# Kernel tuning notes

Hardware: AMD Instinct MI355X
Metric: run time of the kernel (lower is better)

The kernel has to match this reference:

```python
import jax, jax.numpy as jnp
import numpy as np

STRIDE = 1
PADDING = 1

def setup_inputs() -> dict:
    key = jax.random.key(0)
    k1, k2, k3 = jax.random.split(key, 3)
    x = jax.random.normal(k1, (32, 64, 112, 112), dtype=jnp.float32)
    weight = jax.random.normal(k2, (128, 64, 3, 3), dtype=jnp.float32)
    bias = jax.random.normal(k3, (128,), dtype=jnp.float32)
    return {"x": x, "weight": weight, "bias": bias}

def reference(x, weight, bias):
    # Equivalent of the explicit-loop conv: standard cross-correlation conv2d
    # x: [N, C, H, W], weight: [O, C, KH, KW] -> out: [N, O, OH, OW]
    out = jax.lax.conv_general_dilated(
        x, weight,
        window_strides=(STRIDE, STRIDE),
        padding=[(PADDING, PADDING), (PADDING, PADDING)],
        dimension_numbers=("NCHW", "OIHW", "NCHW"),
    )
    return out + bias[None, :, None, None]
```

## Files before the change

kernel.cpp:

```cpp
#include <hip/hip_runtime.h>

#define CIN 64
#define OC 128
#define HW 112
#define HWHW (HW*HW)
#define NIMG 32

#define XN_ELEMS (NIMG*HWHW*CIN)
#define WT_OFF_EL (XN_ELEMS + 128)

#define ROWE (114*64)

typedef __attribute__((ext_vector_type(8))) short short8;
typedef __attribute__((ext_vector_type(4))) float floatx4;

__device__ inline unsigned short f2bf(float f) {
    unsigned u = __float_as_uint(f);
    u += 0x7fffu + ((u >> 16) & 1u);
    return (unsigned short)(u >> 16);
}

__device__ inline void async16(const unsigned short* g, unsigned short* l) {
    __builtin_amdgcn_global_load_lds(
        (const __attribute__((address_space(1))) void*)g,
        (__attribute__((address_space(3))) void*)l, 16, 0, 0);
}

__global__ __launch_bounds__(256) void xform_x(const float* __restrict__ x,
                                               unsigned short* __restrict__ xws)
{
    __shared__ float s[HW * (CIN + 1)];
    const int tid = threadIdx.x;
    const int n = blockIdx.x / HW;
    const int h = blockIdx.x % HW;

    const float* xp = x + (size_t)n * CIN * HWHW + h * HW;
    for (int idx = tid; idx < CIN * HW; idx += 256) {
        int c = idx / HW;
        int w = idx - c * HW;
        s[w * (CIN + 1) + c] = xp[c * HWHW + w];
    }
    __syncthreads();

    unsigned short* op = xws + ((size_t)(n * HW + h)) * HW * CIN;
    for (int idx = tid; idx < (CIN * HW) / 8; idx += 256) {
        int w  = idx >> 3;
        int c0 = (idx & 7) * 8;
        union { unsigned short us[8]; uint4 v; } u;
        #pragma unroll
        for (int j = 0; j < 8; ++j)
            u.us[j] = f2bf(s[w * (CIN + 1) + c0 + j]);
        *(uint4*)(op + w * CIN + c0) = u.v;
    }
}

__global__ __launch_bounds__(256) void xform_w(const float* __restrict__ wgt,
                                               unsigned short* __restrict__ ws16)
{
    const int idx = blockIdx.x * 256 + threadIdx.x;
    const int c = idx & 63;
    const int o = (idx >> 6) & 127;
    const int t = idx >> 13;
    const float v = wgt[(o * CIN + c) * 9 + t];
    ws16[WT_OFF_EL + ((size_t)(t * 2 + (c >> 5)) * 128 + o) * 32 + (c & 31)] = f2bf(v);
}

__global__ __launch_bounds__(256, 2) void conv_mfma(
    const unsigned short* __restrict__ ws16,
    const float* __restrict__ bias,
    float* __restrict__ out)
{
    __shared__ unsigned short sx[4 * ROWE];

    const int tid  = threadIdx.x;
    const int wave = tid >> 6;
    const int lane = tid & 63;
    const int lane_lo = lane & 15;
    const int lane_hi = lane >> 4;

    const int bid = blockIdx.x;
    const int n   = bid / 56;
    const int rp  = bid % 56;
    const int h0  = rp * 2;

    {
        const int slot = wave;
        const int hr = h0 + slot - 1;
        unsigned short* rowb = sx + slot * ROWE;
        if ((unsigned)hr < (unsigned)HW) {
            if (lane < 8)        *(uint4*)(rowb + lane * 8) = (uint4){0,0,0,0};
            else if (lane < 16)  *(uint4*)(rowb + 113*64 + (lane - 8) * 8) = (uint4){0,0,0,0};
            const unsigned short* gr = ws16 + ((size_t)(n * HW + hr)) * HW * CIN;
            const int grp = lane >> 3;
            const int sub = lane & 7;
            const int swz = sub ^ ((1 + grp) & 7);
            const unsigned short* gl = gr + grp * 64 + swz * 8;
            #pragma unroll
            for (int j = 0; j < 14; ++j)
                async16(gl + j * 512, rowb + (1 + j * 8) * 64);
        } else {
            #pragma unroll
            for (int t = 0; t < 14; ++t)
                *(uint4*)(rowb + t * 512 + lane * 8) = (uint4){0,0,0,0};
            if (lane < 16) *(uint4*)(rowb + 7168 + lane * 8) = (uint4){0,0,0,0};
        }
    }
    __syncthreads();

    floatx4 acc[7][4];
    #pragma unroll
    for (int mt = 0; mt < 7; ++mt)
        #pragma unroll
        for (int ot = 0; ot < 4; ++ot)
            acc[mt][ot] = (floatx4){0.f, 0.f, 0.f, 0.f};

    const unsigned short* wA = ws16 + WT_OFF_EL;
    const int row_idx = wave >> 1;
    const int o0 = (wave & 1) * 64;
    const int aL = (o0 + lane_lo) * 32 + lane_hi * 8;

    short8 a[2][2][4];
    #pragma unroll
    for (int k01 = 0; k01 < 2; ++k01)
        #pragma unroll
        for (int ot = 0; ot < 4; ++ot)
            a[0][k01][ot] = *(const short8*)(wA + k01 * 4096 + ot * 512 + aL);

    #pragma unroll
    for (int tap = 0; tap < 9; ++tap) {
        const int dh = tap / 3 - 1;
        const int dw = tap % 3 - 1;
        const int cur = tap & 1, nxt = cur ^ 1;
        if (tap < 8) {
            #pragma unroll
            for (int k01 = 0; k01 < 2; ++k01)
                #pragma unroll
                for (int ot = 0; ot < 4; ++ot)
                    a[nxt][k01][ot] = *(const short8*)(
                        wA + ((tap + 1) * 2 + k01) * 4096 + ot * 512 + aL);
        }
        const int colL = lane_lo + dw + 1;
        const unsigned short* sb = sx + (row_idx + 1 + dh) * ROWE + colL * 64;
        const int sw0 = (lane_hi ^ (colL & 7)) * 8;
        const int sw1 = ((lane_hi + 4) ^ (colL & 7)) * 8;

        #pragma unroll
        for (int mt = 0; mt < 7; ++mt) {
            const short8 b0 = *(const short8*)(sb + mt * 1024 + sw0);
            const short8 b1 = *(const short8*)(sb + mt * 1024 + sw1);
            #pragma unroll
            for (int ot = 0; ot < 4; ++ot)
                acc[mt][ot] = __builtin_amdgcn_mfma_f32_16x16x32_bf16(
                    a[cur][0][ot], b0, acc[mt][ot], 0, 0, 0);
            #pragma unroll
            for (int ot = 0; ot < 4; ++ot)
                acc[mt][ot] = __builtin_amdgcn_mfma_f32_16x16x32_bf16(
                    a[cur][1][ot], b1, acc[mt][ot], 0, 0, 0);
        }
    }

    const int h = h0 + row_idx;
    #pragma unroll
    for (int ot = 0; ot < 4; ++ot) {
        const int ob = o0 + ot * 16 + lane_hi * 4;
        const float4 bv = *(const float4*)(bias + ob);
        #pragma unroll
        for (int mt = 0; mt < 7; ++mt) {
            const int w = mt * 16 + lane_lo;
            float* op = out + ((size_t)(n * OC + ob) * HW + h) * HW + w;
            op[0]        = acc[mt][ot].x + bv.x;
            op[HWHW]     = acc[mt][ot].y + bv.y;
            op[2 * HWHW] = acc[mt][ot].z + bv.z;
            op[3 * HWHW] = acc[mt][ot].w + bv.w;
        }
    }
}

extern "C" void kernel_launch(void* const* d_in, const int* in_sizes, int n_in,
                              void* d_out, int out_size, void* d_ws, size_t ws_size,
                              hipStream_t stream) {
    const float* x    = (const float*)d_in[0];
    const float* wgt  = (const float*)d_in[1];
    const float* bias = (const float*)d_in[2];
    float* out = (float*)d_out;
    unsigned short* ws16 = (unsigned short*)d_ws;

    hipLaunchKernelGGL(xform_x, dim3(NIMG * HW), dim3(256), 0, stream, x, ws16);
    hipLaunchKernelGGL(xform_w, dim3(288), dim3(256), 0, stream, wgt, ws16);
    hipLaunchKernelGGL(conv_mfma, dim3(NIMG * 56), dim3(256), 0, stream,
                       ws16, bias, out);
}
```

Baseline: 332.2 us.

## Process four rows per block with a ring buffer and overlap staging with compute

Each conv block now computes four output rows in two passes over a five-slot LDS ring, so the six input rows it needs are staged once instead of the eight staged by two two-row blocks. The next row's async load and the stores of the first pass run alongside the second pass. Other changes: the x and weight transforms merge into one launch, x reads use float2, block IDs are remapped, and output writes use nontemporal stores. The larger LDS footprint may reduce occupancy, and the extra barriers add synchronisation cost.

```diff
diff --git a/kernel.cpp b/kernel.cpp
--- a/kernel.cpp
+++ b/kernel.cpp
@@ -10,6 +10,7 @@
 #define WT_OFF_EL (XN_ELEMS + 128)
 
 #define ROWE (114*64)
+#define NSLOT 5
 
 typedef __attribute__((ext_vector_type(8))) short short8;
 typedef __attribute__((ext_vector_type(4))) float floatx4;
@@ -26,43 +27,142 @@
         (__attribute__((address_space(3))) void*)l, 16, 0, 0);
 }
 
-__global__ __launch_bounds__(256) void xform_x(const float* __restrict__ x,
-                                               unsigned short* __restrict__ xws)
-{
-    __shared__ float s[HW * (CIN + 1)];
+__global__ __launch_bounds__(256) void xform(const float* __restrict__ x,
+                                             const float* __restrict__ wgt,
+                                             unsigned short* __restrict__ ws16)
+{
     const int tid = threadIdx.x;
-    const int n = blockIdx.x / HW;
-    const int h = blockIdx.x % HW;
-
-    const float* xp = x + (size_t)n * CIN * HWHW + h * HW;
-    for (int idx = tid; idx < CIN * HW; idx += 256) {
-        int c = idx / HW;
-        int w = idx - c * HW;
-        s[w * (CIN + 1) + c] = xp[c * HWHW + w];
-    }
-    __syncthreads();
-
-    unsigned short* op = xws + ((size_t)(n * HW + h)) * HW * CIN;
-    for (int idx = tid; idx < (CIN * HW) / 8; idx += 256) {
-        int w  = idx >> 3;
-        int c0 = (idx & 7) * 8;
-        union { unsigned short us[8]; uint4 v; } u;
-        #pragma unroll
-        for (int j = 0; j < 8; ++j)
-            u.us[j] = f2bf(s[w * (CIN + 1) + c0 + j]);
-        *(uint4*)(op + w * CIN + c0) = u.v;
-    }
-}
-
-__global__ __launch_bounds__(256) void xform_w(const float* __restrict__ wgt,
-                                               unsigned short* __restrict__ ws16)
-{
-    const int idx = blockIdx.x * 256 + threadIdx.x;
-    const int c = idx & 63;
-    const int o = (idx >> 6) & 127;
-    const int t = idx >> 13;
-    const float v = wgt[(o * CIN + c) * 9 + t];
-    ws16[WT_OFF_EL + ((size_t)(t * 2 + (c >> 5)) * 128 + o) * 32 + (c & 31)] = f2bf(v);
+    if (blockIdx.x < NIMG * HW) {
+        __shared__ float s[HW * (CIN + 1)];
+        const int n = blockIdx.x / HW;
+        const int h = blockIdx.x % HW;
+        const float* xp = x + (size_t)n * CIN * HWHW + h * HW;
+        for (int idx = tid; idx < CIN * 56; idx += 256) {
+            const int c  = idx / 56;
+            const int w2 = idx - c * 56;
+            const float2 v = *(const float2*)(xp + c * HWHW + w2 * 2);
+            s[(w2 * 2 + 0) * (CIN + 1) + c] = v.x;
+            s[(w2 * 2 + 1) * (CIN + 1) + c] = v.y;
+        }
+        __syncthreads();
+        unsigned short* op = ws16 + (size_t)(n * HW + h) * HW * CIN;
+        for (int idx = tid; idx < (CIN * HW) / 8; idx += 256) {
+            const int w  = idx >> 3;
+            const int c0 = (idx & 7) * 8;
+            union { unsigned short us[8]; uint4 v; } u;
+            #pragma unroll
+            for (int j = 0; j < 8; ++j)
+                u.us[j] = f2bf(s[w * (CIN + 1) + c0 + j]);
+            *(uint4*)(op + w * CIN + c0) = u.v;
+        }
+    } else {
+        const int idx = (blockIdx.x - NIMG * HW) * 256 + tid;
+        const int c = idx & 63;
+        const int o = (idx >> 6) & 127;
+        const int t = idx >> 13;
+        const float v = wgt[(o * CIN + c) * 9 + t];
+        ws16[WT_OFF_EL + ((size_t)(t * 2 + (c >> 5)) * 128 + o) * 32 + (c & 31)] = f2bf(v);
+    }
+}
+
+__device__ __forceinline__ void stage_row_all(unsigned short* rowb,
+                                              const unsigned short* gr,
+                                              int wave, int lane)
+{
+    if (gr) {
+        const int grp = lane >> 3;
+        const int sub = lane & 7;
+        const int swz = sub ^ ((1 + grp) & 7);
+        const unsigned short* gl = gr + grp * 64 + swz * 8;
+        #pragma unroll
+        for (int k = 0; k < 4; ++k) {
+            const int j = wave + 4 * k;
+            if (j < 14) async16(gl + j * 512, rowb + (1 + j * 8) * 64);
+        }
+        if (wave == 2 && lane < 8) *(uint4*)(rowb + lane * 8) = (uint4){0,0,0,0};
+        if (wave == 3 && lane < 8) *(uint4*)(rowb + 113 * 64 + lane * 8) = (uint4){0,0,0,0};
+    } else {
+        const int t = wave * 64 + lane;
+        #pragma unroll
+        for (int k = 0; k < 4; ++k) {
+            const int e = t + k * 256;
+            if (e < ROWE / 8) *(uint4*)(rowb + e * 8) = (uint4){0,0,0,0};
+        }
+    }
+}
+
+template<int T>
+__device__ __forceinline__ void tile_compute(floatx4 acc[7][4],
+    const unsigned short* __restrict__ wA, const unsigned short* sx,
+    int row_idx, int lane_lo, int lane_hi, int aL)
+{
+    #pragma unroll
+    for (int mt = 0; mt < 7; ++mt)
+        #pragma unroll
+        for (int ot = 0; ot < 4; ++ot)
+            acc[mt][ot] = (floatx4){0.f, 0.f, 0.f, 0.f};
+
+    short8 a[2][2][4];
+    #pragma unroll
+    for (int k01 = 0; k01 < 2; ++k01)
+        #pragma unroll
+        for (int ot = 0; ot < 4; ++ot)
+            a[0][k01][ot] = *(const short8*)(wA + k01 * 4096 + ot * 512 + aL);
+
+    #pragma unroll
+    for (int tap = 0; tap < 9; ++tap) {
+        const int dh = tap / 3 - 1;
+        const int dw = tap % 3 - 1;
+        const int cur = tap & 1, nxt = cur ^ 1;
+        if (tap < 8) {
+            #pragma unroll
+            for (int k01 = 0; k01 < 2; ++k01)
+                #pragma unroll
+                for (int ot = 0; ot < 4; ++ot)
+                    a[nxt][k01][ot] = *(const short8*)(
+                        wA + ((tap + 1) * 2 + k01) * 4096 + ot * 512 + aL);
+        }
+        int slot = row_idx + (1 + dh + 2 * T);
+        if (slot >= NSLOT) slot -= NSLOT;
+        const int colL = lane_lo + dw + 1;
+        const unsigned short* sb = sx + slot * ROWE + colL * 64;
+        const int sw0 = (lane_hi ^ (colL & 7)) * 8;
+        const int sw1 = ((lane_hi + 4) ^ (colL & 7)) * 8;
+
+        #pragma unroll
+        for (int mt = 0; mt < 7; ++mt) {
+            const short8 b0 = *(const short8*)(sb + mt * 1024 + sw0);
+            const short8 b1 = *(const short8*)(sb + mt * 1024 + sw1);
+            #pragma unroll
+            for (int ot = 0; ot < 4; ++ot)
+                acc[mt][ot] = __builtin_amdgcn_mfma_f32_16x16x32_bf16(
+                    a[cur][0][ot], b0, acc[mt][ot], 0, 0, 0);
+            #pragma unroll
+            for (int ot = 0; ot < 4; ++ot)
+                acc[mt][ot] = __builtin_amdgcn_mfma_f32_16x16x32_bf16(
+                    a[cur][1][ot], b1, acc[mt][ot], 0, 0, 0);
+        }
+    }
+}
+
+__device__ __forceinline__ void tile_store(const floatx4 acc[7][4],
+    const float* __restrict__ bias, float* __restrict__ out,
+    int n, int h, int o0, int lane_lo, int lane_hi)
+{
+    #pragma unroll
+    for (int ot = 0; ot < 4; ++ot) {
+        const int ob = o0 + ot * 16 + lane_hi * 4;
+        const float4 bv = *(const float4*)(bias + ob);
+        #pragma unroll
+        for (int mt = 0; mt < 7; ++mt) {
+            const int w = mt * 16 + lane_lo;
+            float* op = out + ((size_t)(n * OC + ob) * HW + h) * HW + w;
+            __builtin_nontemporal_store(acc[mt][ot].x + bv.x, op);
+            __builtin_nontemporal_store(acc[mt][ot].y + bv.y, op + HWHW);
+            __builtin_nontemporal_store(acc[mt][ot].z + bv.z, op + 2 * HWHW);
+            __builtin_nontemporal_store(acc[mt][ot].w + bv.w, op + 3 * HWHW);
+        }
+    }
 }
 
 __global__ __launch_bounds__(256, 2) void conv_mfma(
@@ -70,7 +170,7 @@
     const float* __restrict__ bias,
     float* __restrict__ out)
 {
-    __shared__ unsigned short sx[4 * ROWE];
+    __shared__ unsigned short sx[NSLOT * ROWE];
 
     const int tid  = threadIdx.x;
     const int wave = tid >> 6;
@@ -78,102 +178,46 @@
     const int lane_lo = lane & 15;
     const int lane_hi = lane >> 4;
 
-    const int bid = blockIdx.x;
-    const int n   = bid / 56;
-    const int rp  = bid % 56;
-    const int h0  = rp * 2;
-
-    {
-        const int slot = wave;
-        const int hr = h0 + slot - 1;
-        unsigned short* rowb = sx + slot * ROWE;
-        if ((unsigned)hr < (unsigned)HW) {
-            if (lane < 8)        *(uint4*)(rowb + lane * 8) = (uint4){0,0,0,0};
-            else if (lane < 16)  *(uint4*)(rowb + 113*64 + (lane - 8) * 8) = (uint4){0,0,0,0};
-            const unsigned short* gr = ws16 + ((size_t)(n * HW + hr)) * HW * CIN;
-            const int grp = lane >> 3;
-            const int sub = lane & 7;
-            const int swz = sub ^ ((1 + grp) & 7);
-            const unsigned short* gl = gr + grp * 64 + swz * 8;
-            #pragma unroll
-            for (int j = 0; j < 14; ++j)
-                async16(gl + j * 512, rowb + (1 + j * 8) * 64);
-        } else {
-            #pragma unroll
-            for (int t = 0; t < 14; ++t)
-                *(uint4*)(rowb + t * 512 + lane * 8) = (uint4){0,0,0,0};
-            if (lane < 16) *(uint4*)(rowb + 7168 + lane * 8) = (uint4){0,0,0,0};
-        }
+    const int bid0 = blockIdx.x;
+    const int bid  = (bid0 & 7) * 112 + (bid0 >> 3);
+    const int n  = bid / 28;
+    const int q  = bid - n * 28;
+    const int h0 = q * 4;
+
+    #pragma unroll
+    for (int k = 0; k < 4; ++k) {
+        const int hr = h0 - 1 + k;
+        stage_row_all(sx + k * ROWE,
+                      (hr >= 0) ? ws16 + (size_t)(n * HW + hr) * HW * CIN
+                                : (const unsigned short*)nullptr,
+                      wave, lane);
     }
     __syncthreads();
 
-    floatx4 acc[7][4];
-    #pragma unroll
-    for (int mt = 0; mt < 7; ++mt)
-        #pragma unroll
-        for (int ot = 0; ot < 4; ++ot)
-            acc[mt][ot] = (floatx4){0.f, 0.f, 0.f, 0.f};
+    stage_row_all(sx + 4 * ROWE, ws16 + (size_t)(n * HW + h0 + 3) * HW * CIN,
+                  wave, lane);
 
     const unsigned short* wA = ws16 + WT_OFF_EL;
     const int row_idx = wave >> 1;
     const int o0 = (wave & 1) * 64;
     const int aL = (o0 + lane_lo) * 32 + lane_hi * 8;
 
-    short8 a[2][2][4];
-    #pragma unroll
-    for (int k01 = 0; k01 < 2; ++k01)
-        #pragma unroll
-        for (int ot = 0; ot < 4; ++ot)
-            a[0][k01][ot] = *(const short8*)(wA + k01 * 4096 + ot * 512 + aL);
-
-    #pragma unroll
-    for (int tap = 0; tap < 9; ++tap) {
-        const int dh = tap / 3 - 1;
-        const int dw = tap % 3 - 1;
-        const int cur = tap & 1, nxt = cur ^ 1;
-        if (tap < 8) {
-            #pragma unroll
-            for (int k01 = 0; k01 < 2; ++k01)
-                #pragma unroll
-                for (int ot = 0; ot < 4; ++ot)
-                    a[nxt][k01][ot] = *(const short8*)(
-                        wA + ((tap + 1) * 2 + k01) * 4096 + ot * 512 + aL);
-        }
-        const int colL = lane_lo + dw + 1;
-        const unsigned short* sb = sx + (row_idx + 1 + dh) * ROWE + colL * 64;
-        const int sw0 = (lane_hi ^ (colL & 7)) * 8;
-        const int sw1 = ((lane_hi + 4) ^ (colL & 7)) * 8;
-
-        #pragma unroll
-        for (int mt = 0; mt < 7; ++mt) {
-            const short8 b0 = *(const short8*)(sb + mt * 1024 + sw0);
-            const short8 b1 = *(const short8*)(sb + mt * 1024 + sw1);
-            #pragma unroll
-            for (int ot = 0; ot < 4; ++ot)
-                acc[mt][ot] = __builtin_amdgcn_mfma_f32_16x16x32_bf16(
-                    a[cur][0][ot], b0, acc[mt][ot], 0, 0, 0);
-            #pragma unroll
-            for (int ot = 0; ot < 4; ++ot)
-                acc[mt][ot] = __builtin_amdgcn_mfma_f32_16x16x32_bf16(
-                    a[cur][1][ot], b1, acc[mt][ot], 0, 0, 0);
-        }
-    }
-
-    const int h = h0 + row_idx;
-    #pragma unroll
-    for (int ot = 0; ot < 4; ++ot) {
-        const int ob = o0 + ot * 16 + lane_hi * 4;
-        const float4 bv = *(const float4*)(bias + ob);
-        #pragma unroll
-        for (int mt = 0; mt < 7; ++mt) {
-            const int w = mt * 16 + lane_lo;
-            float* op = out + ((size_t)(n * OC + ob) * HW + h) * HW + w;
-            op[0]        = acc[mt][ot].x + bv.x;
-            op[HWHW]     = acc[mt][ot].y + bv.y;
-            op[2 * HWHW] = acc[mt][ot].z + bv.z;
-            op[3 * HWHW] = acc[mt][ot].w + bv.w;
-        }
-    }
+    floatx4 acc[7][4];
+    tile_compute<0>(acc, wA, sx, row_idx, lane_lo, lane_hi, aL);
+    __syncthreads();
+
+    {
+        const int hr = h0 + 4;
+        stage_row_all(sx + 0 * ROWE,
+                      (hr < HW) ? ws16 + (size_t)(n * HW + hr) * HW * CIN
+                                : (const unsigned short*)nullptr,
+                      wave, lane);
+    }
+    tile_store(acc, bias, out, n, h0 + row_idx, o0, lane_lo, lane_hi);
+    __syncthreads();
+
+    tile_compute<1>(acc, wA, sx, row_idx, lane_lo, lane_hi, aL);
+    tile_store(acc, bias, out, n, h0 + 2 + row_idx, o0, lane_lo, lane_hi);
 }
 
 extern "C" void kernel_launch(void* const* d_in, const int* in_sizes, int n_in,
@@ -185,8 +229,8 @@
     float* out = (float*)d_out;
     unsigned short* ws16 = (unsigned short*)d_ws;
 
-    hipLaunchKernelGGL(xform_x, dim3(NIMG * HW), dim3(256), 0, stream, x, ws16);
-    hipLaunchKernelGGL(xform_w, dim3(288), dim3(256), 0, stream, wgt, ws16);
-    hipLaunchKernelGGL(conv_mfma, dim3(NIMG * 56), dim3(256), 0, stream,
+    hipLaunchKernelGGL(xform, dim3(NIMG * HW + 288), dim3(256), 0, stream,
+                       x, wgt, ws16);
+    hipLaunchKernelGGL(conv_mfma, dim3(896), dim3(256), 0, stream,
                        ws16, bias, out);
 }
```

Measured after the change: 358.0 us. +7.8%, slower.
